# Kernel tuning notes

Hardware: AMD Instinct MI355X
Metric: run time of the kernel (lower is better)

Reference implementation:

```python
import jax, jax.numpy as jnp
import numpy as np

EPS = 1e-7  # eps used inside bbox_iou
LAMBDA_BBOX = 1.0
LAMBDA_CLS = 1.0


def _coords(b):
    x, y, w, h = b[..., 0], b[..., 1], b[..., 2], b[..., 3]
    return x - w / 2, y - h / 2, x + w / 2, y + h / 2


def _pairwise_giou_loss(pred, target):
    # pred [B,T,4] -> [B,T,1,4]; target [B,O,4] -> [B,1,O,4]; broadcast to [B,T,O]
    b1x1, b1y1, b1x2, b1y2 = _coords(pred[:, :, None, :])
    b2x1, b2y1, b2x2, b2y2 = _coords(target[:, None, :, :])
    w1, h1 = b1x2 - b1x1, b1y2 - b1y1 + EPS
    w2, h2 = b2x2 - b2x1, b2y2 - b2y1 + EPS
    inter = jnp.clip(jnp.minimum(b1x2, b2x2) - jnp.maximum(b1x1, b2x1), 0) * \
            jnp.clip(jnp.minimum(b1y2, b2y2) - jnp.maximum(b1y1, b2y1), 0)
    union = w1 * h1 + w2 * h2 - inter + EPS
    iou = inter / union
    cw = jnp.maximum(b1x2, b2x2) - jnp.minimum(b1x1, b2x1)
    ch = jnp.maximum(b1y2, b2y2) - jnp.minimum(b1y1, b2y1)
    c_area = cw * ch + EPS
    giou = iou - (c_area - union) / c_area
    return 1.0 - giou  # [B,T,O]


def _lsa_rows(c):
    # Jonker-Volgenant shortest augmenting path (same algorithm as scipy's
    # linear_sum_assignment). c is [n, m] with n <= m; returns col4row [n].
    n, m = c.shape
    u = np.zeros(n)
    v = np.zeros(m)
    col4row = np.full(n, -1, np.int64)
    row4col = np.full(m, -1, np.int64)
    for cur in range(n):
        shortest = np.full(m, np.inf)
        path = np.full(m, -1, np.int64)
        SR = np.zeros(n, bool)
        SC = np.zeros(m, bool)
        min_val = 0.0
        i = cur
        sink = -1
        while sink == -1:
            SR[i] = True
            r = min_val + c[i] - u[i] - v
            upd = (~SC) & (r < shortest)
            shortest[upd] = r[upd]
            path[upd] = i
            masked = np.where(SC, np.inf, shortest)
            j = int(np.argmin(masked))
            min_val = masked[j]
            SC[j] = True
            if row4col[j] == -1:
                sink = j
            else:
                i = row4col[j]
        u[cur] += min_val
        sr = SR.copy(); sr[cur] = False
        u[sr] += min_val - shortest[col4row[sr]]
        v[SC] -= min_val - shortest[SC]
        j = sink
        while True:
            i = path[j]
            row4col[j] = i
            col4row[i], j = j, col4row[i]
            if i == cur:
                break
    return col4row


def _hungarian_np(cost):
    # Host callback; sequential per-batch like the original scipy loop.
    cost = np.asarray(cost, np.float64)
    B, T, O = cost.shape
    pred_idx = np.zeros((B, O), np.int32)
    tgt_idx = np.zeros((B, O), np.int32)
    for b in range(B):
        col4row = _lsa_rows(cost[b].T)  # assign each target (O rows) a token
        order = np.argsort(col4row)      # sort by pred index like scipy output
        pred_idx[b] = col4row[order].astype(np.int32)
        tgt_idx[b] = order.astype(np.int32)
    return pred_idx, tgt_idx


def _cost_matrix(pred_bboxes, target_bboxes, pred_classes, target_classes):
    B, T, C = pred_classes.shape
    O = target_classes.shape[1]
    log_probs = jax.nn.log_softmax(pred_classes, axis=-1)              # [B,T,C]
    idx = jnp.broadcast_to(target_classes[:, None, :], (B, T, O))      # [B,T,O]
    cls_neg_log = -jnp.take_along_axis(log_probs, idx, axis=-1)        # [B,T,O]
    ciou_loss = _pairwise_giou_loss(pred_bboxes, target_bboxes)        # [B,T,O]
    return LAMBDA_BBOX * ciou_loss + LAMBDA_CLS * cls_neg_log


def setup_inputs() -> dict:
    key = jax.random.key(0)
    k1, k2, k3, k4 = jax.random.split(key, 4)
    B, T, O, C = 32, 2048, 128, 80
    return {
        "pred_bboxes": jax.random.uniform(k1, (B, T, 4), dtype=jnp.float32),
        "target_bboxes": jax.random.uniform(k2, (B, O, 4), dtype=jnp.float32),
        "pred_classes": jax.random.normal(k3, (B, T, C), dtype=jnp.float32),
        "target_classes": jax.random.randint(k4, (B, O), 0, C, dtype=jnp.int32),
    }


def reference(pred_bboxes, target_bboxes, pred_classes, target_classes):
    cost = _cost_matrix(pred_bboxes, target_bboxes, pred_classes, target_classes)
    B, _, O = cost.shape
    out_spec = (jax.ShapeDtypeStruct((B, O), jnp.int32),
                jax.ShapeDtypeStruct((B, O), jnp.int32))
    pred_idx, tgt_idx = jax.pure_callback(_hungarian_np, out_spec, cost)
    return pred_idx, tgt_idx
```

## Files before the change

kernel.cpp:

```cpp
#include <hip/hip_runtime.h>
#include <math.h>
#include <float.h>

#define BB 32
#define TT 2048
#define OO 128
#define CC 80
#define EPSF 1e-7f
#define NT 256
#define SLOTS 8
#define CPAD 81
#define TPT 128
#define NTILE 16

typedef float vf4 __attribute__((ext_vector_type(4)));

struct alignas(16) URow { double u; int row; int pad; };
struct alignas(8)  P2   { int i; int j; };
struct alignas(16) Cand { double v; double u; int j; int row; };

template<int CTRL>
__device__ __forceinline__ void dpp_lexmin(double& bv, int& bj) {
    int lo = __double2loint(bv), hi = __double2hiint(bv);
    int tlo = __builtin_amdgcn_update_dpp(0, lo, CTRL, 0xF, 0xF, false);
    int thi = __builtin_amdgcn_update_dpp(0x7FF00000, hi, CTRL, 0xF, 0xF, false);
    int tj  = __builtin_amdgcn_update_dpp(0x7FFFFFFF, bj, CTRL, 0xF, 0xF, false);
    double tv = __hiloint2double(thi, tlo);
    if (tv <= bv) { bv = tv; bj = tj; }
}

template<int CTRL>
__device__ __forceinline__ void dpp_lexmin_f32(float& bv, int& bj) {
    int tlo = __builtin_amdgcn_update_dpp(0x7F800000, __float_as_int(bv), CTRL, 0xF, 0xF, false);
    int tj  = __builtin_amdgcn_update_dpp(0x7FFFFFFF, bj, CTRL, 0xF, 0xF, false);
    float tv = __int_as_float(tlo);
    if (tv < bv || (tv == bv && tj < bj)) { bv = tv; bj = tj; }
}

struct SMC {
    float  xv[TPT * CPAD];
    float4 box[OO];
    float2 wt[OO];
    unsigned long long rmin[OO * 2];
};

__global__ __launch_bounds__(NT) void hung_cost_kernel(
    const float* __restrict__ pb, const float* __restrict__ tb,
    const float* __restrict__ cls, const int* __restrict__ tcls,
    float* __restrict__ cost, unsigned long long* __restrict__ rowmins) {
#pragma clang fp contract(off)
    __shared__ SMC sm;

    int bx = blockIdx.x;
    int b = bx & 31;
    int tile = bx >> 5;
    int t0 = tile * TPT;
    int tid = threadIdx.x;
    int lane = tid & 63;
    int wave = tid >> 6;
    int tok = tid & (TPT - 1);
    int oh = tid >> 7;

    const float* cbase = cls + ((size_t)b * TT + t0) * CC;
    #pragma unroll
    for (int k = 0; k < (TPT * CC) / (NT * 4); ++k) {
        int idx4 = (k * NT + tid) * 4;
        vf4 vv = __builtin_nontemporal_load((const vf4*)(cbase + idx4));
        int r = idx4 / CC;
        int c = idx4 - r * CC;
        float* dst = &sm.xv[r * CPAD + c];
        dst[0] = vv.x; dst[1] = vv.y; dst[2] = vv.z; dst[3] = vv.w;
    }
    if (tid < OO) {
        float4 tbox = ((const float4*)tb)[b * OO + tid];
        float x1 = tbox.x - tbox.z / 2.f;
        float y1 = tbox.y - tbox.w / 2.f;
        float x2 = tbox.x + tbox.z / 2.f;
        float y2 = tbox.y + tbox.w / 2.f;
        float4 bb; bb.x = x1; bb.y = y1; bb.z = x2; bb.w = y2;
        sm.box[tid] = bb;
        float w2 = x2 - x1;
        float h2 = (y2 - y1) + EPSF;
        float2 wt; wt.x = w2 * h2;
        wt.y = __int_as_float(tcls[b * OO + tid]);
        sm.wt[tid] = wt;
    }
    __syncthreads();

    size_t bt = (size_t)b * TT + t0 + tok;
    float4 pbox = ((const float4*)pb)[bt];
    float b1x1 = pbox.x - pbox.z / 2.f;
    float b1y1 = pbox.y - pbox.w / 2.f;
    float b1x2 = pbox.x + pbox.z / 2.f;
    float b1y2 = pbox.y + pbox.w / 2.f;
    float w1 = b1x2 - b1x1;
    float h1 = (b1y2 - b1y1) + EPSF;
    float w1h1 = w1 * h1;

    const float* xr = &sm.xv[tok * CPAD];
    float m = xr[0];
    #pragma unroll
    for (int c = 1; c < CC; ++c) m = fmaxf(m, xr[c]);
    float ssum = 0.f;
    #pragma unroll
    for (int c = 0; c < CC; ++c) ssum += expf(xr[c] - m);
    float ls = logf(ssum);

    float* cbt = cost + (size_t)b * OO * TT + t0;
    for (int k = 0; k < OO / 2; ++k) {
        int o = oh * (OO / 2) + k;
        float4 bb = sm.box[o];
        float2 wt = sm.wt[o];
        float b2x1 = bb.x, b2y1 = bb.y, b2x2 = bb.z, b2y2 = bb.w;
        float iw = fminf(b1x2, b2x2) - fmaxf(b1x1, b2x1);
        float ih = fminf(b1y2, b2y2) - fmaxf(b1y1, b2y1);
        iw = fmaxf(iw, 0.f);
        ih = fmaxf(ih, 0.f);
        float inter = iw * ih;
        float uni = ((w1h1 + wt.x) - inter) + EPSF;
        float iou = inter / uni;
        float cw = fmaxf(b1x2, b2x2) - fminf(b1x1, b2x1);
        float ch = fmaxf(b1y2, b2y2) - fminf(b1y1, b2y1);
        float c_area = (cw * ch) + EPSF;
        float giou = iou - (c_area - uni) / c_area;
        float bbox_loss = 1.0f - giou;

        float xc = xr[__float_as_int(wt.y)];
        float shifted = xc - m;
        float cls_neg = -(shifted - ls);

        float cval = bbox_loss + cls_neg;
        cbt[(size_t)o * TT + tok] = cval;

        float bvv = cval;
        int bjj = t0 + tok;
        dpp_lexmin_f32<0x111>(bvv, bjj);
        dpp_lexmin_f32<0x112>(bvv, bjj);
        dpp_lexmin_f32<0x114>(bvv, bjj);
        dpp_lexmin_f32<0x118>(bvv, bjj);
        dpp_lexmin_f32<0x142>(bvv, bjj);
        dpp_lexmin_f32<0x143>(bvv, bjj);
        if (lane == 63)
            sm.rmin[o * 2 + (wave & 1)] =
                ((unsigned long long)__float_as_uint(bvv) << 32) | (unsigned)bjj;
    }
    __syncthreads();
    if (tid < OO) {
        unsigned long long r0 = sm.rmin[tid * 2 + 0];
        unsigned long long r1 = sm.rmin[tid * 2 + 1];
        rowmins[((size_t)b * NTILE + tile) * OO + tid] = r0 < r1 ? r0 : r1;
    }
}

struct SML {
    URow   urow[TT];
    P2     path2[TT];
    int    row4col[TT];
    int    claim[TT];
    int    col4row[OO];
    double u[OO];
    int    amin[OO];
    int    flag[OO];
    int    freelist[OO];
    int    selj[OO + 8];
    double selm[OO + 8];
    int    selrow[OO + 8];
    Cand   cand[2][4];
    int    nfree;
};

__global__ __launch_bounds__(NT) void hung_lsa_kernel(
    const float* __restrict__ cost,
    const unsigned long long* __restrict__ rowmins,
    int* __restrict__ out) {
#pragma clang fp contract(off)
    __shared__ SML sm;

    int b = blockIdx.x;
    int tid = threadIdx.x;
    int lane = tid & 63;
    int wave = tid >> 6;

    const float* cb = cost + (size_t)b * OO * TT;
    const int jbase = tid * SLOTS;

    double v_[SLOTS];
    double key[SLOTS];
    #pragma unroll
    for (int s = 0; s < SLOTS; ++s) v_[s] = 0.0;

    if (tid < OO) {
        const unsigned long long* p = rowmins + (size_t)b * NTILE * OO + tid;
        unsigned long long best = p[0];
        #pragma unroll
        for (int t = 1; t < NTILE; ++t) {
            unsigned long long x = p[(size_t)t * OO];
            if (x < best) best = x;
        }
        sm.u[tid] = (double)__uint_as_float((unsigned)(best >> 32));
        sm.amin[tid] = (int)(best & 0xFFFFFFFFull);
        sm.col4row[tid] = -1;
    }
    for (int j = tid; j < TT; j += NT) { sm.row4col[j] = -1; sm.claim[j] = 0x7FFFFFFF; }
    __syncthreads();

    if (tid < OO) atomicMin(&sm.claim[sm.amin[tid]], tid);
    __syncthreads();
    if (tid < OO) {
        int j = sm.amin[tid];
        if (sm.claim[j] == tid) { sm.col4row[tid] = j; sm.row4col[j] = tid; }
    }
    __syncthreads();

    for (int j = tid; j < TT; j += NT) {
        int r = sm.row4col[j];
        URow t; t.row = r; t.u = (r >= 0) ? sm.u[r] : 0.0; t.pad = 0;
        sm.urow[j] = t;
    }
    if (tid < OO) sm.flag[tid] = (sm.col4row[tid] < 0) ? 1 : 0;
    __syncthreads();
    if (tid < OO && sm.flag[tid]) {
        int rank = 0;
        for (int o = 0; o < tid; ++o) rank += sm.flag[o];
        sm.freelist[rank] = tid;
    }
    if (tid == 0) {
        int nf = 0;
        for (int o = 0; o < OO; ++o) nf += sm.flag[o];
        sm.nfree = nf;
    }
    __syncthreads();
    int nfree = sm.nfree;

    float4 pf0, pf1;
    if (nfree > 0) {
        const float* rr = cb + (size_t)sm.freelist[0] * TT + jbase;
        pf0 = *(const float4*)rr;
        pf1 = *(const float4*)(rr + 4);
    }

    int par = 0;
    for (int fi = 0; fi < nfree; ++fi) {
        int cur = sm.freelist[fi];

        #pragma unroll
        for (int s = 0; s < SLOTS; ++s) key[s] = INFINITY;
        int selbits = 0;
        double mv = 0.0;
        int i = cur, jc = -1;
        double ui = sm.u[cur];
        float4 c0 = pf0, c1 = pf1;
        int L = 0, sink;

        while (true) {
            float cv[SLOTS] = {c0.x, c0.y, c0.z, c0.w, c1.x, c1.y, c1.z, c1.w};
            double D = ui - mv;

            double bv = INFINITY;
            int bj = TT;
            #pragma unroll
            for (int s = 0; s < SLOTS; ++s) {
                if (!((selbits >> s) & 1)) {
                    double r = ((double)cv[s] - D) - v_[s];
                    if (r < key[s]) {
                        key[s] = r;
                        P2 p; p.i = i; p.j = jc;
                        sm.path2[s * NT + tid] = p;
                    }
                    double kk = key[s];
                    if (kk < bv) { bv = kk; bj = jbase + s; }
                }
            }
            dpp_lexmin<0x111>(bv, bj);
            dpp_lexmin<0x112>(bv, bj);
            dpp_lexmin<0x114>(bv, bj);
            dpp_lexmin<0x118>(bv, bj);
            dpp_lexmin<0x142>(bv, bj);
            dpp_lexmin<0x143>(bv, bj);
            int rlo = __builtin_amdgcn_readlane(__double2loint(bv), 63);
            int rhi = __builtin_amdgcn_readlane(__double2hiint(bv), 63);
            double wv = __hiloint2double(rhi, rlo);
            int wj = __builtin_amdgcn_readlane(bj, 63);

            URow uwv = sm.urow[wj];

            par ^= 1;
            if (lane == 0) {
                Cand c; c.v = wv; c.u = uwv.u; c.j = wj; c.row = uwv.row;
                sm.cand[par][wave] = c;
            }
            __syncthreads();

            Cand cc0 = sm.cand[par][0];
            Cand cc1 = sm.cand[par][1];
            Cand cc2 = sm.cand[par][2];
            Cand cc3 = sm.cand[par][3];
            double MV = cc0.v; int BJ = cc0.j; int WR = cc0.row; double WU = cc0.u;
            if (cc1.v < MV || (cc1.v == MV && cc1.j < BJ)) { MV = cc1.v; BJ = cc1.j; WR = cc1.row; WU = cc1.u; }
            if (cc2.v < MV || (cc2.v == MV && cc2.j < BJ)) { MV = cc2.v; BJ = cc2.j; WR = cc2.row; WU = cc2.u; }
            if (cc3.v < MV || (cc3.v == MV && cc3.j < BJ)) { MV = cc3.v; BJ = cc3.j; WR = cc3.row; WU = cc3.u; }
            mv = MV;
            if ((BJ >> 3) == tid) selbits |= 1 << (BJ & 7);
            if (tid == 0) sm.selj[L] = BJ;

            if (WR < 0) { sink = BJ; break; }
            if (tid == 0) { sm.selm[L] = MV; sm.selrow[L] = WR; }
            i = WR; ui = WU; jc = BJ;
            L++;
            const float* crow = cb + (size_t)i * TT + jbase;
            c0 = *(const float4*)crow;
            c1 = *(const float4*)(crow + 4);
        }

        if (fi + 1 < nfree) {
            const float* rr = cb + (size_t)sm.freelist[fi + 1] * TT + jbase;
            pf0 = *(const float4*)rr;
            pf1 = *(const float4*)(rr + 4);
        }

        double M = mv;
        #pragma unroll
        for (int s = 0; s < SLOTS; ++s)
            if ((selbits >> s) & 1) v_[s] = v_[s] - (M - key[s]);
        for (int k = tid; k < L; k += NT)
            sm.u[sm.selrow[k]] = sm.u[sm.selrow[k]] + (M - sm.selm[k]);
        if (tid == 0) {
            sm.u[cur] = sm.u[cur] + M;
            int j = sink;
            while (true) {
                P2 p = sm.path2[(j & 7) * NT + (j >> 3)];
                int ii = p.i;
                sm.row4col[j] = ii;
                sm.col4row[ii] = j;
                if (ii == cur) break;
                j = p.j;
            }
        }
        __syncthreads();
        if (tid <= L) {
            int j = sm.selj[tid];
            int r = sm.row4col[j];
            URow t; t.u = sm.u[r]; t.row = r; t.pad = 0;
            sm.urow[j] = t;
        }
        __syncthreads();
    }

    if (tid < OO) {
        int my = sm.col4row[tid];
        int rank = 0;
        for (int o = 0; o < OO; ++o) rank += (sm.col4row[o] < my) ? 1 : 0;
        out[(size_t)b * OO + rank] = my;
        out[(size_t)(BB + b) * OO + rank] = tid;
    }
}

extern "C" void kernel_launch(void* const* d_in, const int* in_sizes, int n_in,
                              void* d_out, int out_size, void* d_ws, size_t ws_size,
                              hipStream_t stream) {
    const float* pred_bboxes = (const float*)d_in[0];
    const float* target_bboxes = (const float*)d_in[1];
    const float* pred_classes = (const float*)d_in[2];
    const int* target_classes = (const int*)d_in[3];
    int* out = (int*)d_out;

    float* cost = (float*)d_ws;
    unsigned long long* rowmins =
        (unsigned long long*)(cost + (size_t)BB * OO * TT);

    hung_cost_kernel<<<BB * NTILE, NT, 0, stream>>>(
        pred_bboxes, target_bboxes, pred_classes, target_classes, cost, rowmins);
    hung_lsa_kernel<<<BB, NT, 0, stream>>>(cost, rowmins, out);
}
```

Measured before the change: 253.6 us.

## Restructure LSA to single-wave search over assigned columns with cached free-column minima

Rewrites the shortest-augmenting-path solver so only one wave runs the per-row search. Instead of scanning all 2048 columns each step, it tracks only the up to 128 assigned columns (two per lane) plus a cached top-2 minimum over unassigned columns per row, whose dual v is still zero. This removes block-wide __syncthreads and the full-width row scans from the inner loop. In exchange it adds the top-2 cache upkeep, occasional 64-lane rescans of a row when its cache runs out, and path reconstruction through lane registers.

```diff
diff --git a/kernel.cpp b/kernel.cpp
--- a/kernel.cpp
+++ b/kernel.cpp
@@ -8,16 +8,13 @@
 #define CC 80
 #define EPSF 1e-7f
 #define NT 256
-#define SLOTS 8
 #define CPAD 81
 #define TPT 128
 #define NTILE 16
+#define INVP 0xFFFFFFFFFFFFFFFFull
 
 typedef float vf4 __attribute__((ext_vector_type(4)));
-
-struct alignas(16) URow { double u; int row; int pad; };
-struct alignas(8)  P2   { int i; int j; };
-struct alignas(16) Cand { double v; double u; int j; int row; };
+typedef unsigned long long u64;
 
 template<int CTRL>
 __device__ __forceinline__ void dpp_lexmin(double& bv, int& bj) {
@@ -26,7 +23,7 @@
     int thi = __builtin_amdgcn_update_dpp(0x7FF00000, hi, CTRL, 0xF, 0xF, false);
     int tj  = __builtin_amdgcn_update_dpp(0x7FFFFFFF, bj, CTRL, 0xF, 0xF, false);
     double tv = __hiloint2double(thi, tlo);
-    if (tv <= bv) { bv = tv; bj = tj; }
+    if (tv < bv || (tv == bv && tj < bj)) { bv = tv; bj = tj; }
 }
 
 template<int CTRL>
@@ -35,6 +32,30 @@
     int tj  = __builtin_amdgcn_update_dpp(0x7FFFFFFF, bj, CTRL, 0xF, 0xF, false);
     float tv = __int_as_float(tlo);
     if (tv < bv || (tv == bv && tj < bj)) { bv = tv; bj = tj; }
+}
+
+template<int CTRL>
+__device__ __forceinline__ void dpp_top2_u64(u64& p1, u64& p2) {
+    int t1lo = __builtin_amdgcn_update_dpp((int)0xFFFFFFFF, (int)(unsigned)(p1 & 0xFFFFFFFFull), CTRL, 0xF, 0xF, false);
+    int t1hi = __builtin_amdgcn_update_dpp((int)0xFFFFFFFF, (int)(unsigned)(p1 >> 32), CTRL, 0xF, 0xF, false);
+    int t2lo = __builtin_amdgcn_update_dpp((int)0xFFFFFFFF, (int)(unsigned)(p2 & 0xFFFFFFFFull), CTRL, 0xF, 0xF, false);
+    int t2hi = __builtin_amdgcn_update_dpp((int)0xFFFFFFFF, (int)(unsigned)(p2 >> 32), CTRL, 0xF, 0xF, false);
+    u64 t1 = ((u64)(unsigned)t1hi << 32) | (unsigned)t1lo;
+    u64 t2 = ((u64)(unsigned)t2hi << 32) | (unsigned)t2lo;
+    if (t1 < p1) { p2 = (p1 < t2) ? p1 : t2; p1 = t1; }
+    else         { p2 = (p2 < t1) ? p2 : t1; }
+}
+
+__device__ __forceinline__ int rl32(int v, int l) { return __builtin_amdgcn_readlane(v, l); }
+__device__ __forceinline__ double rlf64(double v, int l) {
+    int lo = __builtin_amdgcn_readlane(__double2loint(v), l);
+    int hi = __builtin_amdgcn_readlane(__double2hiint(v), l);
+    return __hiloint2double(hi, lo);
+}
+__device__ __forceinline__ u64 rlu64(u64 v, int l) {
+    int lo = __builtin_amdgcn_readlane((int)(unsigned)(v & 0xFFFFFFFFull), l);
+    int hi = __builtin_amdgcn_readlane((int)(unsigned)(v >> 32), l);
+    return ((u64)(unsigned)hi << 32) | (unsigned)lo;
 }
 
 struct SMC {
@@ -153,19 +174,19 @@
 }
 
 struct SML {
-    URow   urow[TT];
-    P2     path2[TT];
     int    row4col[TT];
+    double vcol[TT];
     int    claim[TT];
+    u64    bf2a[OO];
+    u64    bf2b[OO];
+    u64    sc1[NT];
+    u64    sc2[NT];
+    unsigned bitmap[64];
     int    col4row[OO];
     double u[OO];
     int    amin[OO];
     int    flag[OO];
     int    freelist[OO];
-    int    selj[OO + 8];
-    double selm[OO + 8];
-    int    selrow[OO + 8];
-    Cand   cand[2][4];
     int    nfree;
 };
 
@@ -182,19 +203,13 @@
     int wave = tid >> 6;
 
     const float* cb = cost + (size_t)b * OO * TT;
-    const int jbase = tid * SLOTS;
-
-    double v_[SLOTS];
-    double key[SLOTS];
-    #pragma unroll
-    for (int s = 0; s < SLOTS; ++s) v_[s] = 0.0;
 
     if (tid < OO) {
         const unsigned long long* p = rowmins + (size_t)b * NTILE * OO + tid;
         unsigned long long best = p[0];
         #pragma unroll
         for (int t = 1; t < NTILE; ++t) {
-            unsigned long long x = p[(size_t)t * OO];
+            unsigned long long x = p[t * OO];
             if (x < best) best = x;
         }
         sm.u[tid] = (double)__uint_as_float((unsigned)(best >> 32));
@@ -212,13 +227,42 @@
     }
     __syncthreads();
 
-    for (int j = tid; j < TT; j += NT) {
-        int r = sm.row4col[j];
-        URow t; t.row = r; t.u = (r >= 0) ? sm.u[r] : 0.0; t.pad = 0;
-        sm.urow[j] = t;
+    {
+        int prow = tid >> 1, h = tid & 1;
+        const float* rp = cb + (size_t)prow * TT + h * 1024;
+        const int* mrow = &sm.row4col[h * 1024];
+        u64 p1 = INVP, p2 = INVP;
+        for (int k = 0; k < 1024; k += 4) {
+            float4 q = *(const float4*)(rp + k);
+            int4 mm = *(const int4*)(mrow + k);
+            int cbase2 = h * 1024 + k;
+            if (mm.x < 0) { u64 pk = ((u64)__float_as_uint(q.x) << 32) | (unsigned)(cbase2 + 0);
+                            if (pk < p1) { p2 = p1; p1 = pk; } else if (pk < p2) p2 = pk; }
+            if (mm.y < 0) { u64 pk = ((u64)__float_as_uint(q.y) << 32) | (unsigned)(cbase2 + 1);
+                            if (pk < p1) { p2 = p1; p1 = pk; } else if (pk < p2) p2 = pk; }
+            if (mm.z < 0) { u64 pk = ((u64)__float_as_uint(q.z) << 32) | (unsigned)(cbase2 + 2);
+                            if (pk < p1) { p2 = p1; p1 = pk; } else if (pk < p2) p2 = pk; }
+            if (mm.w < 0) { u64 pk = ((u64)__float_as_uint(q.w) << 32) | (unsigned)(cbase2 + 3);
+                            if (pk < p1) { p2 = p1; p1 = pk; } else if (pk < p2) p2 = pk; }
+        }
+        sm.sc1[tid] = p1; sm.sc2[tid] = p2;
+    }
+    for (int j = tid; j < TT; j += NT) sm.vcol[j] = 0.0;
+    if (tid < 64) {
+        unsigned w = 0;
+        for (int k = 0; k < 32; ++k) if (sm.row4col[tid * 32 + k] >= 0) w |= 1u << k;
+        sm.bitmap[tid] = w;
     }
     if (tid < OO) sm.flag[tid] = (sm.col4row[tid] < 0) ? 1 : 0;
     __syncthreads();
+    if (tid < OO) {
+        u64 a1 = sm.sc1[2 * tid], a2 = sm.sc2[2 * tid];
+        u64 b1 = sm.sc1[2 * tid + 1], b2 = sm.sc2[2 * tid + 1];
+        u64 p1, p2;
+        if (a1 < b1) { p1 = a1; p2 = (b1 < a2) ? b1 : a2; }
+        else         { p1 = b1; p2 = (a1 < b2) ? a1 : b2; }
+        sm.bf2a[tid] = p1; sm.bf2b[tid] = p2;
+    }
     if (tid < OO && sm.flag[tid]) {
         int rank = 0;
         for (int o = 0; o < tid; ++o) rank += sm.flag[o];
@@ -230,128 +274,150 @@
         sm.nfree = nf;
     }
     __syncthreads();
+
+    if (wave != 0) return;
+
+    int cid0 = sm.col4row[lane];
+    int cid1 = sm.col4row[lane + 64];
+    double ur0 = sm.u[lane];
+    double ur1 = sm.u[lane + 64];
+    int rpA = 0, rpB = 0, crA = 0, crB = 0;
     int nfree = sm.nfree;
 
-    float4 pf0, pf1;
-    if (nfree > 0) {
-        const float* rr = cb + (size_t)sm.freelist[0] * TT + jbase;
-        pf0 = *(const float4*)rr;
-        pf1 = *(const float4*)(rr + 4);
-    }
-
-    int par = 0;
     for (int fi = 0; fi < nfree; ++fi) {
         int cur = sm.freelist[fi];
-
-        #pragma unroll
-        for (int s = 0; s < SLOTS; ++s) key[s] = INFINITY;
-        int selbits = 0;
-        double mv = 0.0;
-        int i = cur, jc = -1;
-        double ui = sm.u[cur];
-        float4 c0 = pf0, c1 = pf1;
-        int L = 0, sink;
+        double ucur = sm.u[cur];
+        double key0 = INFINITY, key1 = INFINITY;
+        int par0 = 0, par1 = 0;
+        int popped = 0;
+        double mv = 0.0, ui = ucur;
+        int i = cur;
+        double tc = INFINITY; int tcj = 0x7FFFFFFF; int tcpi = cur;
+        int L = 0, sink, spi;
 
         while (true) {
-            float cv[SLOTS] = {c0.x, c0.y, c0.z, c0.w, c1.x, c1.y, c1.z, c1.w};
             double D = ui - mv;
-
-            double bv = INFINITY;
-            int bj = TT;
-            #pragma unroll
-            for (int s = 0; s < SLOTS; ++s) {
-                if (!((selbits >> s) & 1)) {
-                    double r = ((double)cv[s] - D) - v_[s];
-                    if (r < key[s]) {
-                        key[s] = r;
-                        P2 p; p.i = i; p.j = jc;
-                        sm.path2[s * NT + tid] = p;
-                    }
-                    double kk = key[s];
-                    if (kk < bv) { bv = kk; bj = jbase + s; }
+            bool a0 = (cid0 >= 0) && !(popped & 1);
+            bool a1 = (cid1 >= 0) && !(popped & 2);
+            int x0 = a0 ? cid0 : 0;
+            int x1 = a1 ? cid1 : 0;
+            const float* rb = cb + (size_t)i * TT;
+            float cv0 = rb[x0];
+            float cv1 = rb[x1];
+            double vj0 = sm.vcol[x0];
+            double vj1 = sm.vcol[x1];
+            u64 bp = sm.bf2a[i];
+            if (bp == INVP) {
+                unsigned fw = ~sm.bitmap[lane];
+                u64 p1 = INVP, p2 = INVP;
+                const float* rr = rb + lane * 32;
+                for (int k = 0; k < 32; k += 4) {
+                    float4 q = *(const float4*)(rr + k);
+                    int cb2 = lane * 32 + k;
+                    if ((fw >> (k + 0)) & 1) { u64 pk = ((u64)__float_as_uint(q.x) << 32) | (unsigned)(cb2 + 0);
+                        if (pk < p1) { p2 = p1; p1 = pk; } else if (pk < p2) p2 = pk; }
+                    if ((fw >> (k + 1)) & 1) { u64 pk = ((u64)__float_as_uint(q.y) << 32) | (unsigned)(cb2 + 1);
+                        if (pk < p1) { p2 = p1; p1 = pk; } else if (pk < p2) p2 = pk; }
+                    if ((fw >> (k + 2)) & 1) { u64 pk = ((u64)__float_as_uint(q.z) << 32) | (unsigned)(cb2 + 2);
+                        if (pk < p1) { p2 = p1; p1 = pk; } else if (pk < p2) p2 = pk; }
+                    if ((fw >> (k + 3)) & 1) { u64 pk = ((u64)__float_as_uint(q.w) << 32) | (unsigned)(cb2 + 3);
+                        if (pk < p1) { p2 = p1; p1 = pk; } else if (pk < p2) p2 = pk; }
                 }
+                dpp_top2_u64<0x111>(p1, p2);
+                dpp_top2_u64<0x112>(p1, p2);
+                dpp_top2_u64<0x114>(p1, p2);
+                dpp_top2_u64<0x118>(p1, p2);
+                dpp_top2_u64<0x142>(p1, p2);
+                dpp_top2_u64<0x143>(p1, p2);
+                p1 = rlu64(p1, 63); p2 = rlu64(p2, 63);
+                if (lane == 0) { sm.bf2a[i] = p1; sm.bf2b[i] = p2; }
+                bp = p1;
             }
+            {
+                float bfv = __uint_as_float((unsigned)(bp >> 32));
+                int   bfc = (int)(bp & 0xFFFFFFFFull);
+                double cnd = (double)bfv - D;
+                if (cnd < tc || (cnd == tc && bfc < tcj)) { tc = cnd; tcj = bfc; tcpi = i; }
+            }
+            if (a0) { double r = ((double)cv0 - D) - vj0; if (r < key0) { key0 = r; par0 = i; } }
+            if (a1) { double r = ((double)cv1 - D) - vj1; if (r < key1) { key1 = r; par1 = i; } }
+            double bv = INFINITY; int bj = 0x7FFFFFFF;
+            if (a0 && (key0 < bv || (key0 == bv && cid0 < bj))) { bv = key0; bj = cid0; }
+            if (a1 && (key1 < bv || (key1 == bv && cid1 < bj))) { bv = key1; bj = cid1; }
             dpp_lexmin<0x111>(bv, bj);
             dpp_lexmin<0x112>(bv, bj);
             dpp_lexmin<0x114>(bv, bj);
             dpp_lexmin<0x118>(bv, bj);
             dpp_lexmin<0x142>(bv, bj);
             dpp_lexmin<0x143>(bv, bj);
-            int rlo = __builtin_amdgcn_readlane(__double2loint(bv), 63);
-            int rhi = __builtin_amdgcn_readlane(__double2hiint(bv), 63);
-            double wv = __hiloint2double(rhi, rlo);
-            int wj = __builtin_amdgcn_readlane(bj, 63);
-
-            URow uwv = sm.urow[wj];
-
-            par ^= 1;
-            if (lane == 0) {
-                Cand c; c.v = wv; c.u = uwv.u; c.j = wj; c.row = uwv.row;
-                sm.cand[par][wave] = c;
-            }
-            __syncthreads();
-
-            Cand cc0 = sm.cand[par][0];
-            Cand cc1 = sm.cand[par][1];
-            Cand cc2 = sm.cand[par][2];
-            Cand cc3 = sm.cand[par][3];
-            double MV = cc0.v; int BJ = cc0.j; int WR = cc0.row; double WU = cc0.u;
-            if (cc1.v < MV || (cc1.v == MV && cc1.j < BJ)) { MV = cc1.v; BJ = cc1.j; WR = cc1.row; WU = cc1.u; }
-            if (cc2.v < MV || (cc2.v == MV && cc2.j < BJ)) { MV = cc2.v; BJ = cc2.j; WR = cc2.row; WU = cc2.u; }
-            if (cc3.v < MV || (cc3.v == MV && cc3.j < BJ)) { MV = cc3.v; BJ = cc3.j; WR = cc3.row; WU = cc3.u; }
+            double MV = rlf64(bv, 63);
+            int BJ = rl32(bj, 63);
+
+            if (tc < MV || (tc == MV && tcj < BJ)) { sink = tcj; spi = tcpi; break; }
+
             mv = MV;
-            if ((BJ >> 3) == tid) selbits |= 1 << (BJ & 7);
-            if (tid == 0) sm.selj[L] = BJ;
-
-            if (WR < 0) { sink = BJ; break; }
-            if (tid == 0) { sm.selm[L] = MV; sm.selrow[L] = WR; }
-            i = WR; ui = WU; jc = BJ;
-            L++;
-            const float* crow = cb + (size_t)i * TT + jbase;
-            c0 = *(const float4*)crow;
-            c1 = *(const float4*)(crow + 4);
-        }
-
-        if (fi + 1 < nfree) {
-            const float* rr = cb + (size_t)sm.freelist[fi + 1] * TT + jbase;
-            pf0 = *(const float4*)rr;
-            pf1 = *(const float4*)(rr + 4);
-        }
-
-        double M = mv;
-        #pragma unroll
-        for (int s = 0; s < SLOTS; ++s)
-            if ((selbits >> s) & 1) v_[s] = v_[s] - (M - key[s]);
-        for (int k = tid; k < L; k += NT)
-            sm.u[sm.selrow[k]] = sm.u[sm.selrow[k]] + (M - sm.selm[k]);
-        if (tid == 0) {
-            sm.u[cur] = sm.u[cur] + M;
-            int j = sink;
-            while (true) {
-                P2 p = sm.path2[(j & 7) * NT + (j >> 3)];
-                int ii = p.i;
-                sm.row4col[j] = ii;
-                sm.col4row[ii] = j;
-                if (ii == cur) break;
-                j = p.j;
-            }
-        }
-        __syncthreads();
-        if (tid <= L) {
-            int j = sm.selj[tid];
-            int r = sm.row4col[j];
-            URow t; t.u = sm.u[r]; t.row = r; t.pad = 0;
-            sm.urow[j] = t;
-        }
-        __syncthreads();
-    }
-
-    if (tid < OO) {
-        int my = sm.col4row[tid];
+            unsigned long long m0 = __ballot(((popped & 1) == 0) && cid0 == BJ);
+            unsigned long long m1 = __ballot(((popped & 2) == 0) && cid1 == BJ);
+            int ol, os;
+            if (m0) { ol = __ffsll(m0) - 1; os = 0; }
+            else    { ol = __ffsll(m1) - 1; os = 1; }
+            int hrow = os * 64 + ol;
+            double uo = (os == 0) ? rlf64(ur0, ol) : rlf64(ur1, ol);
+            int pp = (os == 0) ? rl32(par0, ol) : rl32(par1, ol);
+            if (lane == ol) popped |= (os ? 2 : 1);
+            int ce = (BJ << 8) | pp;
+            if (L < 64)    { if (lane == L) crA = ce; }
+            else           { if (lane == L - 64) crB = ce; }
+            if (hrow < 64) { if (lane == hrow) rpA = L; }
+            else           { if (lane == hrow - 64) rpB = L; }
+            i = hrow; ui = uo; L++;
+        }
+
+        double M = tc;
+        if (popped & 1) {
+            double d = M - key0; ur0 += d; sm.u[lane] = ur0;
+            double vv = sm.vcol[cid0]; sm.vcol[cid0] = vv - d;
+        }
+        if (popped & 2) {
+            double d = M - key1; ur1 += d; sm.u[lane + 64] = ur1;
+            double vv = sm.vcol[cid1]; sm.vcol[cid1] = vv - d;
+        }
+        int J = sink, ii = spi;
+        while (true) {
+            if (lane == 0) { sm.row4col[J] = ii; sm.col4row[ii] = J; }
+            bool iscur = (ii == cur);
+            if (ii < 64) { if (lane == ii) { cid0 = J; if (iscur) ur0 = ucur + M; } }
+            else         { if (lane == ii - 64) { cid1 = J; if (iscur) ur1 = ucur + M; } }
+            if (iscur) break;
+            int k = (ii < 64) ? rl32(rpA, ii) : rl32(rpB, ii - 64);
+            int ce = (k < 64) ? rl32(crA, k) : rl32(crB, k - 64);
+            J = ce >> 8;
+            ii = ce & 0x7F;
+        }
+        if (lane == 0) {
+            sm.u[cur] = ucur + M;
+            sm.bitmap[sink >> 5] |= 1u << (sink & 31);
+        }
+        {
+            u64 a = sm.bf2a[lane], bb2 = sm.bf2b[lane];
+            if ((unsigned)(a & 0xFFFFFFFFull) == (unsigned)sink) { a = bb2; bb2 = INVP; }
+            else if ((unsigned)(bb2 & 0xFFFFFFFFull) == (unsigned)sink) bb2 = INVP;
+            sm.bf2a[lane] = a; sm.bf2b[lane] = bb2;
+            a = sm.bf2a[lane + 64]; bb2 = sm.bf2b[lane + 64];
+            if ((unsigned)(a & 0xFFFFFFFFull) == (unsigned)sink) { a = bb2; bb2 = INVP; }
+            else if ((unsigned)(bb2 & 0xFFFFFFFFull) == (unsigned)sink) bb2 = INVP;
+            sm.bf2a[lane + 64] = a; sm.bf2b[lane + 64] = bb2;
+        }
+    }
+
+    #pragma unroll
+    for (int h = 0; h < 2; ++h) {
+        int row = lane + h * 64;
+        int my = sm.col4row[row];
         int rank = 0;
         for (int o = 0; o < OO; ++o) rank += (sm.col4row[o] < my) ? 1 : 0;
         out[(size_t)b * OO + rank] = my;
-        out[(size_t)(BB + b) * OO + rank] = tid;
+        out[(size_t)(BB + b) * OO + rank] = row;
     }
 }
 
```

Result: slower. 315.4 us (+24.3%).
